# Performance work log

Hardware: AMD Instinct MI355X
Metric: run time of the kernel (lower is better)

Reference implementation:

```python
import jax, jax.numpy as jnp
import numpy as np

N_NODES = 50000
N_EDGES = 800000
IN_DIM = 256
HEADS = 4
HEAD_DIM = 64  # out_dim // heads
NEG_SLOPE = 0.2  # PyG GATConv default


def setup_inputs() -> dict:
    key = jax.random.key(0)
    k1, k2, k3, k4, k5 = jax.random.split(key, 5)
    x = jax.random.normal(k1, (N_NODES, IN_DIM), dtype=jnp.float32)
    edge_index = jax.random.randint(k2, (2, N_EDGES), 0, N_NODES, dtype=jnp.int64)
    # Glorot-ish scaling
    W = jax.random.normal(k3, (IN_DIM, HEADS * HEAD_DIM), dtype=jnp.float32) * (1.0 / np.sqrt(IN_DIM))
    att_src = jax.random.normal(k4, (HEADS, HEAD_DIM), dtype=jnp.float32) * (1.0 / np.sqrt(HEAD_DIM))
    att_dst = jax.random.normal(k5, (HEADS, HEAD_DIM), dtype=jnp.float32) * (1.0 / np.sqrt(HEAD_DIM))
    bias = jnp.zeros((HEADS * HEAD_DIM,), dtype=jnp.float32)
    return {"x": x, "edge_index": edge_index, "W": W, "att_src": att_src,
            "att_dst": att_dst, "bias": bias}


def reference(x, edge_index, W, att_src, att_dst, bias):
    N = x.shape[0]
    # add self-loops (PyG GATConv default)
    loops = jnp.arange(N, dtype=edge_index.dtype)
    src = jnp.concatenate([edge_index[0], loops])
    dst = jnp.concatenate([edge_index[1], loops])

    h = (x @ W).reshape(N, HEADS, HEAD_DIM)          # [N,H,D]
    a_src = jnp.einsum('nhd,hd->nh', h, att_src)     # [N,H]
    a_dst = jnp.einsum('nhd,hd->nh', h, att_dst)     # [N,H]

    e = a_src[src] + a_dst[dst]                      # [E,H]
    e = jax.nn.leaky_relu(e, NEG_SLOPE)

    # segment softmax over edges sharing a destination node
    m = jax.ops.segment_max(e, dst, num_segments=N)  # [N,H]
    e = jnp.exp(e - m[dst])
    denom = jax.ops.segment_sum(e, dst, num_segments=N)  # [N,H]
    alpha = e / denom[dst]                           # [E,H]

    msg = alpha[:, :, None] * h[src]                 # [E,H,D]
    out = jax.ops.segment_sum(msg, dst, num_segments=N)  # [N,H,D]
    return out.reshape(N, HEADS * HEAD_DIM) + bias
```

## Files before the change

### kernel.cpp

```cpp
#include <hip/hip_runtime.h>
#include <hip/hip_bf16.h>

#define N_NODES 50000
#define N_EDGES 800000
#define IN_DIM 256
#define HEADS 4
#define HEAD_DIM 64
#define OUT_DIM 256
#define NEG_SLOPE 0.2f
#define TOTAL_E (N_EDGES + N_NODES)
#define M_PAD 50048
#define SEG_CAP 64

#define GEMM_BLOCKS 782
#define SCAT_BLOCKS 3321
#define MEGA_BLOCKS (GEMM_BLOCKS + SCAT_BLOCKS)

typedef float floatx4 __attribute__((ext_vector_type(4)));
typedef short shortx8 __attribute__((ext_vector_type(8)));

__global__ __launch_bounds__(256) void prep_wt(const float* __restrict__ W,
                                               ushort* __restrict__ Wt) {
    int t = blockIdx.x * 256 + threadIdx.x;
    int n = t >> 6;
    int k = (t & 63) << 2;
    ushort4 o;
    o.x = __bfloat16_as_ushort(__float2bfloat16(W[(size_t)(k + 0) * OUT_DIM + n]));
    o.y = __bfloat16_as_ushort(__float2bfloat16(W[(size_t)(k + 1) * OUT_DIM + n]));
    o.z = __bfloat16_as_ushort(__float2bfloat16(W[(size_t)(k + 2) * OUT_DIM + n]));
    o.w = __bfloat16_as_ushort(__float2bfloat16(W[(size_t)(k + 3) * OUT_DIM + n]));
    *(ushort4*)&Wt[(size_t)n * IN_DIM + k] = o;
}

__global__ __launch_bounds__(256) void mega_kernel(const float* __restrict__ x,
                                                   const ushort* __restrict__ Wt,
                                                   const float* __restrict__ att_src,
                                                   const float* __restrict__ att_dst,
                                                   const int* __restrict__ e_src,
                                                   const int* __restrict__ e_dst,
                                                   int* __restrict__ cnt,
                                                   int* __restrict__ csr,
                                                   ushort* __restrict__ h2,
                                                   float* __restrict__ asrc,
                                                   float* __restrict__ adst) {
    if (blockIdx.x >= GEMM_BLOCKS) {
        int id = (blockIdx.x - GEMM_BLOCKS) * 256 + threadIdx.x;
        if (id < N_EDGES) {
            int s = e_src[id];
            int dn = e_dst[id];
            int pos = atomicAdd(&cnt[dn], 1);
            if (pos < SEG_CAP) csr[(dn << 6) + pos] = s;
        } else if (id < TOTAL_E) {
            int nn = id - N_EDGES;
            int pos = atomicAdd(&cnt[nn], 1);
            if (pos < SEG_CAP) csr[(nn << 6) + pos] = nn;
        }
        return;
    }

    const int tid = threadIdx.x;
    const int w = tid >> 6;
    const int lane = tid & 63;
    const int quad = lane >> 4;
    const int l16 = lane & 15;
    const int row0 = blockIdx.x * 64;

    floatx4 acc[4][4] = {};

    const ushort* wtb = Wt + (size_t)(w * 64 + l16) * IN_DIM + quad * 8;

#pragma unroll 2
    for (int k0 = 0; k0 < IN_DIM; k0 += 32) {
        shortx8 bfr[4], af[4];
#pragma unroll
        for (int c = 0; c < 4; ++c)
            bfr[c] = *(const shortx8*)(wtb + (size_t)c * 16 * IN_DIM + k0);
#pragma unroll
        for (int r = 0; r < 4; ++r) {
            int gr = row0 + r * 16 + l16;
            alignas(16) ushort a8[8];
            if (gr < N_NODES) {
                const float* xp = &x[(size_t)gr * IN_DIM + k0 + quad * 8];
                float4 v0 = *(const float4*)xp;
                float4 v1 = *(const float4*)(xp + 4);
                float f[8] = {v0.x, v0.y, v0.z, v0.w, v1.x, v1.y, v1.z, v1.w};
#pragma unroll
                for (int u = 0; u < 8; ++u)
                    a8[u] = __bfloat16_as_ushort(__float2bfloat16(f[u]));
            } else {
#pragma unroll
                for (int u = 0; u < 8; ++u) a8[u] = 0;
            }
            af[r] = *(const shortx8*)a8;
        }
#pragma unroll
        for (int r = 0; r < 4; ++r)
#pragma unroll
            for (int c = 0; c < 4; ++c)
                acc[r][c] = __builtin_amdgcn_mfma_f32_16x16x32_bf16(bfr[c], af[r],
                                                                    acc[r][c], 0, 0, 0);
    }

    float as_cj[16], ad_cj[16];
#pragma unroll
    for (int c = 0; c < 4; ++c)
#pragma unroll
        for (int j = 0; j < 4; ++j) {
            int col = w * 64 + c * 16 + quad * 4 + j;
            as_cj[c * 4 + j] = att_src[col];
            ad_cj[c * 4 + j] = att_dst[col];
        }
#pragma unroll
    for (int r = 0; r < 4; ++r) {
        float s = 0.f, d = 0.f;
        alignas(16) ushort o16[16];
#pragma unroll
        for (int c = 0; c < 4; ++c)
#pragma unroll
            for (int j = 0; j < 4; ++j) {
                float v = acc[r][c][j];
                s = fmaf(v, as_cj[c * 4 + j], s);
                d = fmaf(v, ad_cj[c * 4 + j], d);
                o16[c * 4 + j] = __bfloat16_as_ushort(__float2bfloat16(v));
            }
        s += __shfl_xor(s, 16);
        s += __shfl_xor(s, 32);
        d += __shfl_xor(d, 16);
        d += __shfl_xor(d, 32);
        int gr = row0 + r * 16 + l16;
        if (quad == 0 && gr < N_NODES) {
            asrc[gr * HEADS + w] = s;
            adst[gr * HEADS + w] = d;
        }
        ushort* hp = h2 + (size_t)gr * OUT_DIM + w * 64 + quad * 16;
        *(uint4*)hp = *(const uint4*)&o16[0];
        *(uint4*)(hp + 8) = *(const uint4*)&o16[8];
    }
}

__global__ __launch_bounds__(256) void aggregate_v8(const uint2* __restrict__ h2,
                                                    const float* __restrict__ a_src,
                                                    const float* __restrict__ a_dst,
                                                    const int* __restrict__ cnt,
                                                    const int* __restrict__ csr,
                                                    const float* __restrict__ bias,
                                                    float* __restrict__ out) {
    int n = blockIdx.x * 4 + (threadIdx.x >> 6);
    if (n >= N_NODES) return;
    int lane = threadIdx.x & 63;
    int h = lane >> 4;
    int col0 = ((lane >> 4) << 6) + ((lane & 3) << 4) + (((lane >> 2) & 3) << 2);
    int beg = n << 6;
    int cn = min(cnt[n], SEG_CAP);
    int nfull = cn >> 3, rem = cn & 7;
    float adv = a_dst[n * HEADS + h];

    float den = 0.f;
    float acc0 = 0.f, acc1 = 0.f, acc2 = 0.f, acc3 = 0.f;
    for (int b = 0; b < nfull; ++b) {
        int i = beg + b * 8;
        int4 sa = *(const int4*)&csr[i];
        int4 sb = *(const int4*)&csr[i + 4];
        int ss[8] = {sa.x, sa.y, sa.z, sa.w, sb.x, sb.y, sb.z, sb.w};
        float asv[8];
        uint2 hv[8];
#pragma unroll
        for (int u = 0; u < 8; ++u) {
            asv[u] = a_src[ss[u] * HEADS + h];
            hv[u] = h2[(size_t)ss[u] * 64 + lane];
        }
#pragma unroll
        for (int u = 0; u < 8; ++u) {
            float e = asv[u] + adv;
            e = fmaxf(e, NEG_SLOPE * e);
            float p = __expf(e);
            den += p;
            acc0 = fmaf(p, __uint_as_float(hv[u].x << 16), acc0);
            acc1 = fmaf(p, __uint_as_float(hv[u].x & 0xffff0000u), acc1);
            acc2 = fmaf(p, __uint_as_float(hv[u].y << 16), acc2);
            acc3 = fmaf(p, __uint_as_float(hv[u].y & 0xffff0000u), acc3);
        }
    }
    if (rem) {
        int i = beg + nfull * 8;
        int4 sa = *(const int4*)&csr[i];
        int4 sb = *(const int4*)&csr[i + 4];
        int ss[8] = {sa.x, sa.y, sa.z, sa.w, sb.x, sb.y, sb.z, sb.w};
        float asv[8];
        uint2 hv[8];
#pragma unroll
        for (int u = 0; u < 8; ++u) {
            int s = (u < rem) ? ss[u] : 0;
            asv[u] = a_src[s * HEADS + h];
            hv[u] = h2[(size_t)s * 64 + lane];
        }
#pragma unroll
        for (int u = 0; u < 8; ++u) {
            float e = asv[u] + adv;
            e = fmaxf(e, NEG_SLOPE * e);
            float p = (u < rem) ? __expf(e) : 0.f;
            den += p;
            acc0 = fmaf(p, __uint_as_float(hv[u].x << 16), acc0);
            acc1 = fmaf(p, __uint_as_float(hv[u].x & 0xffff0000u), acc1);
            acc2 = fmaf(p, __uint_as_float(hv[u].y << 16), acc2);
            acc3 = fmaf(p, __uint_as_float(hv[u].y & 0xffff0000u), acc3);
        }
    }
    float idv = 1.0f / den;
    float4 b = *(const float4*)&bias[col0];
    float4 o = make_float4(acc0 * idv + b.x, acc1 * idv + b.y,
                           acc2 * idv + b.z, acc3 * idv + b.w);
    *(float4*)&out[(size_t)n * OUT_DIM + col0] = o;
}

extern "C" void kernel_launch(void* const* d_in, const int* in_sizes, int n_in,
                              void* d_out, int out_size, void* d_ws, size_t ws_size,
                              hipStream_t stream) {
    const float* x = (const float*)d_in[0];
    const int* ei = (const int*)d_in[1];
    const float* W = (const float*)d_in[2];
    const float* att_src = (const float*)d_in[3];
    const float* att_dst = (const float*)d_in[4];
    const float* bias = (const float*)d_in[5];
    float* out = (float*)d_out;

    const int* e_src = ei;
    const int* e_dst = ei + N_EDGES;

    char* p = (char*)d_ws;
    auto alloc = [&](size_t bytes) {
        void* r = (void*)p;
        p += (bytes + 255) & ~(size_t)255;
        return r;
    };
    ushort* h2   = (ushort*)alloc((size_t)M_PAD * OUT_DIM * 2);
    float* asrc  = (float*)alloc((size_t)N_NODES * HEADS * 4);
    float* adst  = (float*)alloc((size_t)N_NODES * HEADS * 4);
    int* cnt     = (int*)alloc((size_t)N_NODES * 4);
    int* csr     = (int*)alloc((size_t)N_NODES * SEG_CAP * 4);
    ushort* Wt   = (ushort*)alloc((size_t)IN_DIM * OUT_DIM * 2);

    hipMemsetAsync(cnt, 0, (size_t)N_NODES * 4, stream);
    prep_wt<<<64, 256, 0, stream>>>(W, Wt);
    mega_kernel<<<MEGA_BLOCKS, 256, 0, stream>>>(x, Wt, att_src, att_dst, e_src, e_dst,
                                                 cnt, csr, h2, asrc, adst);
    aggregate_v8<<<(N_NODES + 3) / 4, 256, 0, stream>>>((const uint2*)h2, asrc, adst,
                                                        cnt, csr, bias, out);
}
```

Before: 245.9 us.

## Stage GEMM A tiles via async global-to-LDS double buffering and fold memset into prep

The GEMM part of the mega kernel now loads x tiles into a swizzled, double-buffered LDS area using global_load_lds, prefetching the next K-slice while the current one feeds MFMAs. This replaces per-lane direct global float4 loads that each wave issued redundantly for its rows. The cnt zeroing memset is merged into the weight-transpose prep kernel, saving one launch. In exchange it adds 16KB of LDS per block (also reserved by the scatter blocks) and a barrier per K step, which may lower occupancy.

```diff
diff --git a/kernel.cpp b/kernel.cpp
--- a/kernel.cpp
+++ b/kernel.cpp
@@ -19,18 +19,26 @@
 typedef float floatx4 __attribute__((ext_vector_type(4)));
 typedef short shortx8 __attribute__((ext_vector_type(8)));
 
-__global__ __launch_bounds__(256) void prep_wt(const float* __restrict__ W,
-                                               ushort* __restrict__ Wt) {
-    int t = blockIdx.x * 256 + threadIdx.x;
-    int n = t >> 6;
-    int k = (t & 63) << 2;
-    ushort4 o;
-    o.x = __bfloat16_as_ushort(__float2bfloat16(W[(size_t)(k + 0) * OUT_DIM + n]));
-    o.y = __bfloat16_as_ushort(__float2bfloat16(W[(size_t)(k + 1) * OUT_DIM + n]));
-    o.z = __bfloat16_as_ushort(__float2bfloat16(W[(size_t)(k + 2) * OUT_DIM + n]));
-    o.w = __bfloat16_as_ushort(__float2bfloat16(W[(size_t)(k + 3) * OUT_DIM + n]));
-    *(ushort4*)&Wt[(size_t)n * IN_DIM + k] = o;
-}
+__global__ __launch_bounds__(256) void prep(const float* __restrict__ W,
+                                            ushort* __restrict__ Wt,
+                                            int* __restrict__ cnt) {
+    int b = blockIdx.x;
+    if (b < 64) {
+        int t = b * 256 + threadIdx.x;
+        int n = t >> 6;
+        int k = (t & 63) << 2;
+        ushort4 o;
+        o.x = __bfloat16_as_ushort(__float2bfloat16(W[(size_t)(k + 0) * OUT_DIM + n]));
+        o.y = __bfloat16_as_ushort(__float2bfloat16(W[(size_t)(k + 1) * OUT_DIM + n]));
+        o.z = __bfloat16_as_ushort(__float2bfloat16(W[(size_t)(k + 2) * OUT_DIM + n]));
+        o.w = __bfloat16_as_ushort(__float2bfloat16(W[(size_t)(k + 3) * OUT_DIM + n]));
+        *(ushort4*)&Wt[(size_t)n * IN_DIM + k] = o;
+    } else {
+        int t = (b - 64) * 256 + threadIdx.x;
+        if (t < 12500) ((int4*)cnt)[t] = make_int4(0, 0, 0, 0);
+    }
+}
+#define PREP_BLOCKS 113
 
 __global__ __launch_bounds__(256) void mega_kernel(const float* __restrict__ x,
                                                    const ushort* __restrict__ Wt,
@@ -43,6 +51,8 @@
                                                    ushort* __restrict__ h2,
                                                    float* __restrict__ asrc,
                                                    float* __restrict__ adst) {
+    __shared__ float A_lds[2][64 * 32];
+
     if (blockIdx.x >= GEMM_BLOCKS) {
         int id = (blockIdx.x - GEMM_BLOCKS) * 256 + threadIdx.x;
         if (id < N_EDGES) {
@@ -65,32 +75,48 @@
     const int l16 = lane & 15;
     const int row0 = blockIdx.x * 64;
 
+    auto stage = [&](int buf, int k0) {
+#pragma unroll
+        for (int i = 0; i < 2; ++i) {
+            int s = i * 256 + tid;
+            int row = s >> 3;
+            int cg = (s & 7) ^ (row & 7);
+            int gr = row0 + row;
+            if (gr > N_NODES - 1) gr = N_NODES - 1;
+            const float* src = &x[(size_t)gr * IN_DIM + k0 + cg * 4];
+            __builtin_amdgcn_global_load_lds(
+                (const __attribute__((address_space(1))) unsigned int*)src,
+                (__attribute__((address_space(3))) unsigned int*)&A_lds[buf][s * 4],
+                16, 0, 0);
+        }
+    };
+
     floatx4 acc[4][4] = {};
-
     const ushort* wtb = Wt + (size_t)(w * 64 + l16) * IN_DIM + quad * 8;
 
+    stage(0, 0);
+    __syncthreads();
 #pragma unroll 2
-    for (int k0 = 0; k0 < IN_DIM; k0 += 32) {
+    for (int t = 0; t < 8; ++t) {
+        int cur = t & 1;
+        if (t < 7) stage(cur ^ 1, (t + 1) * 32);
+        int k0 = t * 32;
         shortx8 bfr[4], af[4];
 #pragma unroll
         for (int c = 0; c < 4; ++c)
             bfr[c] = *(const shortx8*)(wtb + (size_t)c * 16 * IN_DIM + k0);
 #pragma unroll
         for (int r = 0; r < 4; ++r) {
-            int gr = row0 + r * 16 + l16;
+            int row = r * 16 + l16;
+            const float* Ab = &A_lds[cur][row * 32];
+            int sw = row & 7;
+            float4 f0 = *(const float4*)&Ab[((2 * quad) ^ sw) * 4];
+            float4 f1 = *(const float4*)&Ab[((2 * quad + 1) ^ sw) * 4];
+            float f[8] = {f0.x, f0.y, f0.z, f0.w, f1.x, f1.y, f1.z, f1.w};
             alignas(16) ushort a8[8];
-            if (gr < N_NODES) {
-                const float* xp = &x[(size_t)gr * IN_DIM + k0 + quad * 8];
-                float4 v0 = *(const float4*)xp;
-                float4 v1 = *(const float4*)(xp + 4);
-                float f[8] = {v0.x, v0.y, v0.z, v0.w, v1.x, v1.y, v1.z, v1.w};
-#pragma unroll
-                for (int u = 0; u < 8; ++u)
-                    a8[u] = __bfloat16_as_ushort(__float2bfloat16(f[u]));
-            } else {
-#pragma unroll
-                for (int u = 0; u < 8; ++u) a8[u] = 0;
-            }
+#pragma unroll
+            for (int u = 0; u < 8; ++u)
+                a8[u] = __bfloat16_as_ushort(__float2bfloat16(f[u]));
             af[r] = *(const shortx8*)a8;
         }
 #pragma unroll
@@ -99,6 +125,7 @@
             for (int c = 0; c < 4; ++c)
                 acc[r][c] = __builtin_amdgcn_mfma_f32_16x16x32_bf16(bfr[c], af[r],
                                                                     acc[r][c], 0, 0, 0);
+        __syncthreads();
     }
 
     float as_cj[16], ad_cj[16];
@@ -240,8 +267,7 @@
     int* csr     = (int*)alloc((size_t)N_NODES * SEG_CAP * 4);
     ushort* Wt   = (ushort*)alloc((size_t)IN_DIM * OUT_DIM * 2);
 
-    hipMemsetAsync(cnt, 0, (size_t)N_NODES * 4, stream);
-    prep_wt<<<64, 256, 0, stream>>>(W, Wt);
+    prep<<<PREP_BLOCKS, 256, 0, stream>>>(W, Wt, cnt);
     mega_kernel<<<MEGA_BLOCKS, 256, 0, stream>>>(x, Wt, att_src, att_dst, e_src, e_dst,
                                                  cnt, csr, h2, asrc, adst);
     aggregate_v8<<<(N_NODES + 3) / 4, 256, 0, stream>>>((const uint2*)h2, asrc, adst,
```

After: 226.4 us. 1.09x faster.
